# Optimization experiments

Measured on AMD Instinct MI355X. Metric: run time of the kernel, lower is better.

## Reference

```python
import jax, jax.numpy as jnp
import numpy as np

B_, L_, H_ = 8, 512, 768
DIN, N, R, K = 1536, 64, 48, 4  # d_inner, d_state, dt_rank, d_conv


def setup_inputs() -> dict:
    key = jax.random.key(0)
    ks = jax.random.split(key, 16)
    rn = lambda i, shp, sc=0.02: jax.random.normal(ks[i], shp, dtype=jnp.float32) * sc
    inp = {
        "text": jax.random.normal(ks[0], (B_, L_, H_), dtype=jnp.float32),
        "audio": jax.random.normal(ks[1], (B_, L_, H_), dtype=jnp.float32),
        "video": jax.random.normal(ks[2], (B_, L_, H_), dtype=jnp.float32),
        "proj_w": rn(3, (3 * H_, H_)),
        "proj_b": jnp.zeros((H_,), jnp.float32),
        "proj_ln_g": jnp.ones((H_,), jnp.float32),
        "proj_ln_b": jnp.zeros((H_,), jnp.float32),
        "blk_ln_g": jnp.ones((H_,), jnp.float32),
        "blk_ln_b": jnp.zeros((H_,), jnp.float32),
        "in_proj_w": rn(4, (H_, 2 * DIN)),
        "conv_w": rn(5, (DIN, 1, K), 0.1),
        "conv_b": jnp.zeros((DIN,), jnp.float32),
        "x_proj_w": rn(6, (DIN, R + 2 * N)),
        "dt_proj_w": rn(7, (R, DIN), 0.1),
        "dt_proj_b": jnp.full((DIN,), -4.6, jnp.float32),  # softplus -> ~0.01 dt
        "A_log": jnp.log(jnp.tile(jnp.arange(1, N + 1, dtype=jnp.float32), (DIN, 1))),
        "D": jnp.ones((DIN,), jnp.float32),
        "out_proj_w": rn(8, (DIN, H_)),
    }
    return inp


def _ln(x, g, b, eps=1e-5):
    mu = x.mean(-1, keepdims=True)
    xc = x - mu
    v = (xc * xc).mean(-1, keepdims=True)
    return xc * jax.lax.rsqrt(v + eps) * g + b


def _mamba(h, in_proj_w, conv_w, conv_b, x_proj_w, dt_proj_w, dt_proj_b, A_log, D, out_proj_w):
    Bsz, L, _ = h.shape
    xz = h @ in_proj_w                       # [B,L,2*DIN]
    x, z = jnp.split(xz, 2, axis=-1)         # each [B,L,DIN]
    # causal depthwise conv1d over time
    xc = jax.lax.conv_general_dilated(
        x.transpose(0, 2, 1), conv_w, (1,), [(K - 1, 0)],
        dimension_numbers=("NCH", "OIH", "NCH"), feature_group_count=DIN)
    x = jax.nn.silu(xc + conv_b[None, :, None]).transpose(0, 2, 1)  # [B,L,DIN]
    dbl = x @ x_proj_w                       # [B,L,R+2N]
    dt, Bm, Cm = jnp.split(dbl, [R, R + N], axis=-1)
    delta = jax.nn.softplus(dt @ dt_proj_w + dt_proj_b)  # [B,L,DIN]
    A = -jnp.exp(A_log)                      # [DIN,N]

    def step(hcar, t):
        d_t, b_t, c_t, u_t = t               # [B,DIN],[B,N],[B,N],[B,DIN]
        hcar = jnp.exp(d_t[..., None] * A) * hcar + (d_t * u_t)[..., None] * b_t[:, None, :]
        y = jnp.einsum("bdn,bn->bd", hcar, c_t)
        return hcar, y

    xs = (delta.transpose(1, 0, 2), Bm.transpose(1, 0, 2), Cm.transpose(1, 0, 2), x.transpose(1, 0, 2))
    h0 = jnp.zeros((Bsz, DIN, N), x.dtype)
    _, ys = jax.lax.scan(step, h0, xs)       # ys: [L,B,DIN]
    y = ys.transpose(1, 0, 2) + x * D
    y = y * jax.nn.silu(z)
    return y @ out_proj_w                    # [B,L,H]


def reference(text, audio, video, proj_w, proj_b, proj_ln_g, proj_ln_b,
              blk_ln_g, blk_ln_b, in_proj_w, conv_w, conv_b, x_proj_w,
              dt_proj_w, dt_proj_b, A_log, D, out_proj_w):
    fused = jnp.concatenate([text, audio, video], axis=-1) @ proj_w + proj_b
    fused = _ln(fused, proj_ln_g, proj_ln_b)
    m = _mamba(_ln(fused, blk_ln_g, blk_ln_b), in_proj_w, conv_w, conv_b,
               x_proj_w, dt_proj_w, dt_proj_b, A_log, D, out_proj_w)
    fused = fused + m                         # residual (dropout = identity in eval)
    return fused.mean(axis=1)                 # [B,H]
```

## Files before the change

kernel.cpp:

```cpp
#include <hip/hip_runtime.h>
#include <hip/hip_bf16.h>
#include <cstddef>
#include <cstdint>

#define DIN 1536
#define LSEQ 512

typedef __hip_bfloat16 bf16;
typedef __attribute__((ext_vector_type(8))) short short8x;
typedef __attribute__((ext_vector_type(4))) float f32x4;
typedef const __attribute__((address_space(1))) unsigned int* gp1;
typedef __attribute__((address_space(3))) unsigned int* lp3;

__device__ inline float readlane_f(float v, int l) {
  return __uint_as_float(__builtin_amdgcn_readlane(__float_as_uint(v), l));
}
__device__ inline void gload_lds(const bf16* g, unsigned short* l) {
  __builtin_amdgcn_global_load_lds((gp1)g, (lp3)l, 16, 0, 0);
}
__device__ inline void bsplit(float v, bf16& h, bf16& l) {
  h = __float2bfloat16(v);
  l = __float2bfloat16(v - __bfloat162float(h));
}
__device__ inline float softplusf(float t) {
  return fmaxf(t, 0.f) + log1pf(__expf(-fabsf(t)));
}
template<int CTRL>
__device__ inline float dpp_add(float v) {
  int t = __builtin_amdgcn_update_dpp(0, __float_as_int(v), CTRL, 0xf, 0xf, true);
  return v + __int_as_float(t);
}
__device__ inline float dpp_wave_sum(float p) {
  p = dpp_add<0x111>(p);
  p = dpp_add<0x112>(p);
  p = dpp_add<0x114>(p);
  p = dpp_add<0x118>(p);
  p = dpp_add<0x142>(p);
  p = dpp_add<0x143>(p);
  return p;
}

template<int TBM, int TBN, int WR, int WC, int AMODE, int EPI>
__global__ __launch_bounds__(WR*WC*64) void mgemm(
    const bf16* __restrict__ Ah0, const bf16* __restrict__ Al0,
    const bf16* __restrict__ Ah1, const bf16* __restrict__ Al1,
    const bf16* __restrict__ Ah2, const bf16* __restrict__ Al2,
    const bf16* __restrict__ Bh, const bf16* __restrict__ Bl,
    const float* __restrict__ bias,
    float* __restrict__ C, float* __restrict__ C2,
    bf16* __restrict__ Oh, bf16* __restrict__ Ol,
    int K, int lda, int ldc)
{
  constexpr int NW = WR * WC;
  constexpr int SM = TBM / WR, SN = TBN / WC;
  constexpr int T_M = SM / 16, T_N = SN / 16;
  __shared__ unsigned short sAh[TBM * 32], sAl[TBM * 32];
  __shared__ unsigned short sBh[TBN * 32], sBl[TBN * 32];
  const int tid = threadIdx.x;
  const int lane = tid & 63, wid = tid >> 6;
  const int bm = blockIdx.x * TBM, bn = blockIdx.y * TBN;
  const int wr = wid / WC, wc = wid % WC;

  const int stg_m = lane >> 2;
  const int stg_k = ((lane & 3) ^ ((lane >> 3) & 3)) * 8;
  const int fo = (lane & 15) * 64 + ((((lane >> 4) ^ ((lane >> 1) & 3)) & 3) * 16);

  f32x4 acc[T_M][T_N];
  #pragma unroll
  for (int i = 0; i < T_M; ++i)
    #pragma unroll
    for (int j = 0; j < T_N; ++j) acc[i][j] = (f32x4){0.f, 0.f, 0.f, 0.f};

  for (int k0 = 0; k0 < K; k0 += 32) {
    __syncthreads();
    const bf16* pAh; const bf16* pAl; int ka;
    if (AMODE == 1) {
      int seg = k0 / 768;
      pAh = (seg == 0) ? Ah0 : (seg == 1) ? Ah1 : Ah2;
      pAl = (seg == 0) ? Al0 : (seg == 1) ? Al1 : Al2;
      ka = k0 - seg * 768;
    } else { pAh = Ah0; pAl = Al0; ka = k0; }
    #pragma unroll
    for (int q = wid; q < TBM / 16; q += NW) {
      size_t go = (size_t)(bm + q * 16 + stg_m) * lda + ka + stg_k;
      gload_lds(pAh + go, &sAh[q * 512]);
      gload_lds(pAl + go, &sAl[q * 512]);
    }
    #pragma unroll
    for (int q = wid; q < TBN / 16; q += NW) {
      size_t go = (size_t)(bn + q * 16 + stg_m) * K + k0 + stg_k;
      gload_lds(Bh + go, &sBh[q * 512]);
      gload_lds(Bl + go, &sBl[q * 512]);
    }
    __syncthreads();

    short8x ah[T_M], al[T_M], bh[T_N], bl[T_N];
    #pragma unroll
    for (int mi = 0; mi < T_M; ++mi) {
      int off = (wr * SM + mi * 16) * 64 + fo;
      ah[mi] = *(const short8x*)((const char*)sAh + off);
      al[mi] = *(const short8x*)((const char*)sAl + off);
    }
    #pragma unroll
    for (int nj = 0; nj < T_N; ++nj) {
      int off = (wc * SN + nj * 16) * 64 + fo;
      bh[nj] = *(const short8x*)((const char*)sBh + off);
      bl[nj] = *(const short8x*)((const char*)sBl + off);
    }
    #pragma unroll
    for (int mi = 0; mi < T_M; ++mi)
      #pragma unroll
      for (int nj = 0; nj < T_N; ++nj) {
        acc[mi][nj] = __builtin_amdgcn_mfma_f32_16x16x32_bf16(ah[mi], bh[nj], acc[mi][nj], 0, 0, 0);
        acc[mi][nj] = __builtin_amdgcn_mfma_f32_16x16x32_bf16(ah[mi], bl[nj], acc[mi][nj], 0, 0, 0);
        acc[mi][nj] = __builtin_amdgcn_mfma_f32_16x16x32_bf16(al[mi], bh[nj], acc[mi][nj], 0, 0, 0);
      }
  }

  const int cl = lane & 15, qd = lane >> 4;
  const int colbase = bn + wc * SN;
  const int rowbase = bm + wr * SM;
  if (EPI == 1) {
    #pragma unroll
    for (int mi = 0; mi < T_M; ++mi) {
      int r0 = rowbase + mi * 16 + qd * 4;
      #pragma unroll
      for (int nj = 0; nj < T_N; ++nj) {
        int col = colbase + nj * 16 + cl;
        float bv = bias[col];
        #pragma unroll
        for (int rg = 0; rg < 4; ++rg)
          C[(size_t)(r0 + rg) * ldc + col] = acc[mi][nj][rg] + bv;
      }
    }
  } else if (EPI == 4) {
    #pragma unroll
    for (int mi = 0; mi < T_M; ++mi) {
      int m = rowbase + mi * 16 + qd * 4;
      int b = m >> 9, l = m & 511;
      #pragma unroll
      for (int nj = 0; nj < T_N; ++nj) {
        int col = colbase + nj * 16 + cl;
        float bv = bias[col];
        float4 v;
        v.x = softplusf(acc[mi][nj][0] + bv);
        v.y = softplusf(acc[mi][nj][1] + bv);
        v.z = softplusf(acc[mi][nj][2] + bv);
        v.w = softplusf(acc[mi][nj][3] + bv);
        *reinterpret_cast<float4*>(&C[((size_t)b * DIN + col) * LSEQ + l]) = v;
      }
    }
  } else if (EPI == 5) {
    if (bn < 1536) {
      #pragma unroll
      for (int mi = 0; mi < T_M; ++mi) {
        int r0 = rowbase + mi * 16 + qd * 4;
        #pragma unroll
        for (int nj = 0; nj < T_N; ++nj) {
          int col = colbase + nj * 16 + cl;
          #pragma unroll
          for (int rg = 0; rg < 4; ++rg)
            C[(size_t)(r0 + rg) * ldc + col] = acc[mi][nj][rg];
        }
      }
    } else {
      #pragma unroll
      for (int mi = 0; mi < T_M; ++mi) {
        int m = rowbase + mi * 16 + qd * 4;
        int b = m >> 9, l = m & 511;
        #pragma unroll
        for (int nj = 0; nj < T_N; ++nj) {
          int colz = colbase - 1536 + nj * 16 + cl;
          float4 v;
          v.x = acc[mi][nj][0]; v.y = acc[mi][nj][1];
          v.z = acc[mi][nj][2]; v.w = acc[mi][nj][3];
          *reinterpret_cast<float4*>(&C2[((size_t)b * DIN + colz) * LSEQ + l]) = v;
        }
      }
    }
  } else if (EPI == 6) {
    #pragma unroll
    for (int mi = 0; mi < T_M; ++mi) {
      int r0 = rowbase + mi * 16 + qd * 4;
      #pragma unroll
      for (int nj = 0; nj < T_N; ++nj) {
        int col = colbase + nj * 16 + cl;
        #pragma unroll
        for (int rg = 0; rg < 4; ++rg) {
          float v = acc[mi][nj][rg];
          C[(size_t)(r0 + rg) * 192 + col] = v;
          if (col < 64) {
            bf16 h, l;
            if (col < 48) bsplit(v, h, l);
            else { h = __float2bfloat16(0.f); l = h; }
            Oh[(size_t)(r0 + rg) * 64 + col] = h;
            Ol[(size_t)(r0 + rg) * 64 + col] = l;
          }
        }
      }
    }
  }
}

__global__ __launch_bounds__(256) void prep_k(
    const float* __restrict__ s0, const float* __restrict__ s1,
    const float* __restrict__ s2, bf16* __restrict__ moddst,
    const float* __restrict__ pw, const float* __restrict__ ipw,
    const float* __restrict__ xpw, const float* __restrict__ dtw,
    bf16* pwTh, bf16* pwTl, bf16* ipTh, bf16* ipTl,
    bf16* xpTh, bf16* xpTl, bf16* dtTh, bf16* dtTl)
{
  __shared__ float T[64][65];
  const int tid = threadIdx.x;
  if (blockIdx.x < 36864) {
    const int per = 4096 * 768 / 256;
    int seg = blockIdx.x / per;
    int idx = (blockIdx.x - seg * per) * 256 + tid;
    const float* src = (seg == 0) ? s0 : (seg == 1) ? s1 : s2;
    bf16* hi = moddst + (size_t)seg * 2 * 4096 * 768;
    bf16* lo = hi + (size_t)4096 * 768;
    bf16 h, l; bsplit(src[idx], h, l);
    hi[idx] = h; lo[idx] = l;
    return;
  }
  const int id = blockIdx.x - 36864;
  const float* src; bf16 *hi, *lo; int P, Q, ld, Ppad, px, qx;
  if (id < 432)       { src = pw;  hi = pwTh; lo = pwTl; P = 2304; Q = 768;  ld = 768;  Ppad = 2304; px = id % 36;          qx = id / 36; }
  else if (id < 1008) { int i = id - 432;  src = ipw; hi = ipTh; lo = ipTl; P = 768;  Q = 3072; ld = 3072; Ppad = 768;  px = i % 12; qx = i / 12; }
  else if (id < 1080) { int i = id - 1008; src = xpw; hi = xpTh; lo = xpTl; P = 1536; Q = 176;  ld = 176;  Ppad = 1536; px = i % 24; qx = i / 24; }
  else                { int i = id - 1080; src = dtw; hi = dtTh; lo = dtTl; P = 48;   Q = 1536; ld = 1536; Ppad = 64;   px = 0;      qx = i; }
  const int p0 = px * 64, q0 = qx * 64;
  {
    int j = tid & 63, i0 = tid >> 6;
    for (int i = i0; i < 64; i += 4) {
      int p = p0 + i, q = q0 + j;
      T[i][j] = (p < P && q < Q) ? src[(size_t)p * ld + q] : 0.f;
    }
  }
  __syncthreads();
  {
    int ii = tid & 63, j0 = tid >> 6;
    for (int jj = j0; jj < 64; jj += 4) {
      bf16 h, l; bsplit(T[ii][jj], h, l);
      size_t o = (size_t)(q0 + jj) * Ppad + p0 + ii;
      hi[o] = h; lo[o] = l;
    }
  }
}

__device__ inline float block_sum256(float s, float* red) {
  #pragma unroll
  for (int o = 32; o > 0; o >>= 1) s += __shfl_xor(s, o, 64);
  int tid = threadIdx.x;
  __syncthreads();
  if ((tid & 63) == 0) red[tid >> 6] = s;
  __syncthreads();
  return red[0] + red[1] + red[2] + red[3];
}

__global__ __launch_bounds__(256) void ln2_k(
    const float* __restrict__ pre,
    const float* __restrict__ g1, const float* __restrict__ b1,
    const float* __restrict__ g2, const float* __restrict__ b2,
    float* __restrict__ fused, bf16* __restrict__ hAh, bf16* __restrict__ hAl)
{
  __shared__ float red[4];
  const int row = blockIdx.x;
  const int tid = threadIdx.x;
  const float* x = pre + (size_t)row * 768;
  float v0 = x[tid], v1 = x[tid + 256], v2 = x[tid + 512];

  float mu = block_sum256(v0 + v1 + v2, red) * (1.f / 768.f);
  float c0 = v0 - mu, c1 = v1 - mu, c2 = v2 - mu;
  float var = block_sum256(c0*c0 + c1*c1 + c2*c2, red) * (1.f / 768.f);
  float r = rsqrtf(var + 1e-5f);
  float f0 = c0 * r * g1[tid] + b1[tid];
  float f1 = c1 * r * g1[tid + 256] + b1[tid + 256];
  float f2 = c2 * r * g1[tid + 512] + b1[tid + 512];
  float* fo = fused + (size_t)row * 768;
  fo[tid] = f0; fo[tid + 256] = f1; fo[tid + 512] = f2;

  float mu2 = block_sum256(f0 + f1 + f2, red) * (1.f / 768.f);
  float d0 = f0 - mu2, d1 = f1 - mu2, d2 = f2 - mu2;
  float var2 = block_sum256(d0*d0 + d1*d1 + d2*d2, red) * (1.f / 768.f);
  float r2 = rsqrtf(var2 + 1e-5f);
  float h0 = d0 * r2 * g2[tid] + b2[tid];
  float h1 = d1 * r2 * g2[tid + 256] + b2[tid + 256];
  float h2 = d2 * r2 * g2[tid + 512] + b2[tid + 512];
  bf16 hh, hl;
  size_t o = (size_t)row * 768;
  bsplit(h0, hh, hl); hAh[o + tid] = hh; hAl[o + tid] = hl;
  bsplit(h1, hh, hl); hAh[o + tid + 256] = hh; hAl[o + tid + 256] = hl;
  bsplit(h2, hh, hl); hAh[o + tid + 512] = hh; hAl[o + tid + 512] = hl;
}

__global__ __launch_bounds__(256) void conv2x_k(
    const float* __restrict__ xbuf, const float* __restrict__ w,
    const float* __restrict__ cb, float* __restrict__ xct,
    bf16* __restrict__ xcAh, bf16* __restrict__ xcAl)
{
  __shared__ float Xs[67][65];
  __shared__ float Ys[64][65];
  const int tid = threadIdx.x;
  const int l0 = blockIdx.x * 64;
  const int d0 = blockIdx.y * 64;
  const int b  = blockIdx.z;
  for (int e = tid; e < 67 * 64; e += 256) {
    int r = e >> 6, dd = e & 63;
    int l = l0 - 3 + r;
    Xs[r][dd] = (l >= 0) ? xbuf[((size_t)b * 512 + l) * DIN + d0 + dd] : 0.f;
  }
  __syncthreads();
  {
    const int lane = tid & 63, grp = tid >> 6;
    #pragma unroll
    for (int i = 0; i < 16; ++i) {
      int dd = grp + i * 4;
      int d = d0 + dd;
      float acc = cb[d];
      #pragma unroll
      for (int k = 0; k < 4; ++k)
        acc = fmaf(Xs[lane + k][dd], w[d * 4 + k], acc);
      float v = acc / (1.f + __expf(-acc));
      xct[((size_t)b * DIN + d) * LSEQ + l0 + lane] = v;
      Ys[lane][dd] = v;
    }
  }
  __syncthreads();
  {
    const int dd = tid & 63, lg = tid >> 6;
    #pragma unroll
    for (int j = 0; j < 16; ++j) {
      int l = lg * 16 + j;
      bf16 h, lo; bsplit(Ys[l][dd], h, lo);
      size_t o = (size_t)(b * 512 + l0 + l) * DIN + d0 + dd;
      xcAh[o] = h; xcAl[o] = lo;
    }
  }
}

__global__ __launch_bounds__(256) void scan5_k(
    const float* __restrict__ delta_t, const float* __restrict__ xct,
    const float* __restrict__ dbl, const float* __restrict__ zt,
    const float* __restrict__ A_log, const float* __restrict__ Dv,
    float* __restrict__ ysbar)
{
  __shared__ float BC[64][128];
  __shared__ float DT[4][64][2];
  __shared__ float Pq[4][64][17];
  const int tid = threadIdx.x;
  const int lane = tid & 63;
  const int wv = tid >> 6;
  const int bid = blockIdx.x;
  const int b = bid / 384;
  const int d = (bid - b * 384) * 4 + wv;
  const float Ad2 = -__expf(A_log[d * 64 + lane]) * 1.442695041f;
  const float Dd = Dv[d];
  const size_t strm = ((size_t)b * DIN + d) * LSEQ;
  float h = 0.f, ysum = 0.f;

  for (int l0 = 0; l0 < LSEQ; l0 += 64) {
    __syncthreads();
    #pragma unroll
    for (int i = 0; i < 16; ++i) {
      int t = wv * 16 + i;
      const float* src = dbl + (size_t)(b * LSEQ + l0 + t) * 192;
      float2 v; v.x = src[48 + lane]; v.y = src[112 + lane];
      *reinterpret_cast<float2*>(&BC[t][lane * 2]) = v;
    }
    float dt_v = delta_t[strm + l0 + lane];
    float u_v  = xct[strm + l0 + lane];
    float z_v  = zt[strm + l0 + lane];
    float2 dd; dd.x = dt_v; dd.y = dt_v * u_v;
    *reinterpret_cast<float2*>(&DT[wv][lane][0]) = dd;
    __syncthreads();

    #pragma unroll
    for (int t = 0; t < 64; ++t) {
      float2 sd = *reinterpret_cast<const float2*>(&DT[wv][t][0]);
      float2 bc = *reinterpret_cast<const float2*>(&BC[t][lane * 2]);
      float e = exp2f(sd.x * Ad2);
      h = fmaf(e, h, sd.y * bc.x);
      float p = h * bc.y;
      p = dpp_add<0x111>(p);
      p = dpp_add<0x112>(p);
      if ((lane & 3) == 3) Pq[wv][t][lane >> 2] = p;
    }
    float yk = 0.f;
    #pragma unroll
    for (int j = 0; j < 16; ++j) yk += Pq[wv][lane][j];
    float yv = (yk + u_v * Dd) * (z_v / (1.f + __expf(-z_v)));
    ysum += yv;
  }
  float tot = readlane_f(dpp_wave_sum(ysum), 63);
  if (lane == 0) ysbar[b * 1536 + d] = tot;
}

__global__ __launch_bounds__(256) void final_k(
    const float* __restrict__ fused, const float* __restrict__ ysbar,
    const float* __restrict__ W, float* __restrict__ out)
{
  __shared__ float ys[1536];
  const int b = blockIdx.y;
  const int c = blockIdx.x * 256 + threadIdx.x;
  for (int i = threadIdx.x; i < 1536; i += 256) ys[i] = ysbar[b * 1536 + i];
  __syncthreads();
  float sf = 0.f;
  for (int l = 0; l < 512; ++l) sf += fused[(size_t)((b << 9) + l) * 768 + c];
  float dot = 0.f;
  for (int d = 0; d < 1536; ++d) dot = fmaf(ys[d], W[(size_t)d * 768 + c], dot);
  out[b * 768 + c] = (sf + dot) * (1.f / 512.f);
}

extern "C" void kernel_launch(void* const* d_in, const int* in_sizes, int n_in,
                              void* d_out, int out_size, void* d_ws, size_t ws_size,
                              hipStream_t stream)
{
  const float* text      = (const float*)d_in[0];
  const float* audio     = (const float*)d_in[1];
  const float* video     = (const float*)d_in[2];
  const float* proj_w    = (const float*)d_in[3];
  const float* proj_b    = (const float*)d_in[4];
  const float* proj_ln_g = (const float*)d_in[5];
  const float* proj_ln_b = (const float*)d_in[6];
  const float* blk_ln_g  = (const float*)d_in[7];
  const float* blk_ln_b  = (const float*)d_in[8];
  const float* in_proj_w = (const float*)d_in[9];
  const float* conv_w    = (const float*)d_in[10];
  const float* conv_b    = (const float*)d_in[11];
  const float* x_proj_w  = (const float*)d_in[12];
  const float* dt_proj_w = (const float*)d_in[13];
  const float* dt_proj_b = (const float*)d_in[14];
  const float* A_log     = (const float*)d_in[15];
  const float* Dv        = (const float*)d_in[16];
  const float* out_projw = (const float*)d_in[17];
  float* out = (float*)d_out;

  char* p = (char*)d_ws;
  const size_t P768 = (size_t)4096 * 768 * 2;
  char* S1 = p; p += 6 * P768;
  char* SW = p; p += 18087936;
  char* S3 = p; p += (size_t)4096 * 768 * 4;
  char* S4 = p; p += (size_t)4096 * 768 * 4;
  char* S6 = p; p += (size_t)4096 * 1536 * 4;
  char* S7 = p; p += (size_t)4096 * 1536 * 4;
  char* S8 = p; p += (size_t)4096 * 1536 * 4;
  char* SD = p; p += (size_t)4096 * 64 * 4;
  char* S9 = p; p += (size_t)4096 * 192 * 4;
  char* SY = p; p += 12288 * 4;

  bf16* modspl = (bf16*)S1;
  bf16 *tAh = (bf16*)S1,              *tAl = (bf16*)(S1 + P768);
  bf16 *aAh = (bf16*)(S1 + 2 * P768), *aAl = (bf16*)(S1 + 3 * P768);
  bf16 *vAh = (bf16*)(S1 + 4 * P768), *vAl = (bf16*)(S1 + 5 * P768);
  bf16 *hAh = (bf16*)S1,              *hAl = (bf16*)(S1 + P768);
  bf16 *xcAh = (bf16*)S1,             *xcAl = (bf16*)(S1 + (size_t)4096 * 1536 * 2);
  bf16 *pwTh = (bf16*)SW,                    *pwTl = pwTh + (size_t)768 * 2304;
  bf16 *ipTh = pwTl + (size_t)768 * 2304,    *ipTl = ipTh + (size_t)3072 * 768;
  bf16 *xpTh = ipTl + (size_t)3072 * 768,    *xpTl = xpTh + (size_t)192 * 1536;
  bf16 *dtTh = xpTl + (size_t)192 * 1536,    *dtTl = dtTh + (size_t)1536 * 64;
  float* pre     = (float*)S3;
  float* fused   = (float*)S4;
  float* xbuf    = (float*)S6;  float* delta_t = (float*)S6;
  float* zt      = (float*)S7;
  float* xct     = (float*)S8;
  bf16 *dtAh = (bf16*)SD, *dtAl = (bf16*)(SD + (size_t)4096 * 64 * 2);
  float* dbl     = (float*)S9;
  float* ysbar   = (float*)SY;

  prep_k<<<37968, 256, 0, stream>>>(text, audio, video, modspl,
                                    proj_w, in_proj_w, x_proj_w, dt_proj_w,
                                    pwTh, pwTl, ipTh, ipTl, xpTh, xpTl, dtTh, dtTl);
  mgemm<128, 64, 4, 2, 1, 1><<<dim3(32, 12), 512, 0, stream>>>(
      tAh, tAl, aAh, aAl, vAh, vAl, pwTh, pwTl, proj_b,
      pre, nullptr, nullptr, nullptr, 2304, 768, 768);
  ln2_k<<<4096, 256, 0, stream>>>(pre, proj_ln_g, proj_ln_b, blk_ln_g, blk_ln_b, fused, hAh, hAl);
  mgemm<128, 128, 2, 2, 0, 5><<<dim3(32, 24), 256, 0, stream>>>(
      hAh, hAl, nullptr, nullptr, nullptr, nullptr, ipTh, ipTl, nullptr,
      xbuf, zt, nullptr, nullptr, 768, 768, 1536);
  conv2x_k<<<dim3(8, 24, 8), 256, 0, stream>>>(xbuf, conv_w, conv_b, xct, xcAh, xcAl);
  mgemm<64, 64, 4, 2, 0, 6><<<dim3(64, 3), 512, 0, stream>>>(
      xcAh, xcAl, nullptr, nullptr, nullptr, nullptr, xpTh, xpTl, nullptr,
      dbl, nullptr, dtAh, dtAl, 1536, 1536, 192);
  mgemm<128, 64, 4, 2, 0, 4><<<dim3(32, 24), 512, 0, stream>>>(
      dtAh, dtAl, nullptr, nullptr, nullptr, nullptr, dtTh, dtTl, dt_proj_b,
      delta_t, nullptr, nullptr, nullptr, 64, 64, 0);
  scan5_k<<<3072, 256, 0, stream>>>(delta_t, xct, dbl, zt, A_log, Dv, ysbar);
  final_k<<<dim3(3, 8), 256, 0, stream>>>(fused, ysbar, out_projw, out);
}
```

Before: 663.7 us.

## Fold gate and time-sum into scan accumulator, drop per-step y reduction

The scan kernel no longer builds y_t per timestep through DPP reductions and an LDS transpose. It uses linearity of the time-mean: each lane accumulates h*C*silu(z) directly into one scalar, and the wave is reduced once at the end. The per-step dt, dt*u and gate scalars are broadcast with readlane instead of LDS reads. Blocks grow to 8 waves so the B/C tile loaded into LDS is shared by more channels. The cost is a different summation order, plus three readlanes and an extra multiply per step.

```diff
diff --git a/kernel.cpp b/kernel.cpp
--- a/kernel.cpp
+++ b/kernel.cpp
@@ -339,31 +339,31 @@
   }
 }
 
-__global__ __launch_bounds__(256) void scan5_k(
+__global__ __launch_bounds__(512) void scan6_k(
     const float* __restrict__ delta_t, const float* __restrict__ xct,
     const float* __restrict__ dbl, const float* __restrict__ zt,
     const float* __restrict__ A_log, const float* __restrict__ Dv,
     float* __restrict__ ysbar)
 {
   __shared__ float BC[64][128];
-  __shared__ float DT[4][64][2];
-  __shared__ float Pq[4][64][17];
   const int tid = threadIdx.x;
   const int lane = tid & 63;
   const int wv = tid >> 6;
   const int bid = blockIdx.x;
-  const int b = bid / 384;
-  const int d = (bid - b * 384) * 4 + wv;
+  const int b = bid / 192;
+  const int d = (bid - b * 192) * 8 + wv;
   const float Ad2 = -__expf(A_log[d * 64 + lane]) * 1.442695041f;
   const float Dd = Dv[d];
   const size_t strm = ((size_t)b * DIN + d) * LSEQ;
-  float h = 0.f, ysum = 0.f;
+  float h = 0.f;
+  float a = 0.f;
+  float us = 0.f;
 
   for (int l0 = 0; l0 < LSEQ; l0 += 64) {
     __syncthreads();
     #pragma unroll
-    for (int i = 0; i < 16; ++i) {
-      int t = wv * 16 + i;
+    for (int i = 0; i < 8; ++i) {
+      int t = wv * 8 + i;
       const float* src = dbl + (size_t)(b * LSEQ + l0 + t) * 192;
       float2 v; v.x = src[48 + lane]; v.y = src[112 + lane];
       *reinterpret_cast<float2*>(&BC[t][lane * 2]) = v;
@@ -371,28 +371,23 @@
     float dt_v = delta_t[strm + l0 + lane];
     float u_v  = xct[strm + l0 + lane];
     float z_v  = zt[strm + l0 + lane];
-    float2 dd; dd.x = dt_v; dd.y = dt_v * u_v;
-    *reinterpret_cast<float2*>(&DT[wv][lane][0]) = dd;
+    float du_v = dt_v * u_v;
+    float sz_v = z_v / (1.f + __expf(-z_v));
+    us += u_v * sz_v;
     __syncthreads();
 
     #pragma unroll
     for (int t = 0; t < 64; ++t) {
-      float2 sd = *reinterpret_cast<const float2*>(&DT[wv][t][0]);
+      float sdt = readlane_f(dt_v, t);
+      float sdu = readlane_f(du_v, t);
+      float ssz = readlane_f(sz_v, t);
       float2 bc = *reinterpret_cast<const float2*>(&BC[t][lane * 2]);
-      float e = exp2f(sd.x * Ad2);
-      h = fmaf(e, h, sd.y * bc.x);
-      float p = h * bc.y;
-      p = dpp_add<0x111>(p);
-      p = dpp_add<0x112>(p);
-      if ((lane & 3) == 3) Pq[wv][t][lane >> 2] = p;
-    }
-    float yk = 0.f;
-    #pragma unroll
-    for (int j = 0; j < 16; ++j) yk += Pq[wv][lane][j];
-    float yv = (yk + u_v * Dd) * (z_v / (1.f + __expf(-z_v)));
-    ysum += yv;
-  }
-  float tot = readlane_f(dpp_wave_sum(ysum), 63);
+      float e = exp2f(sdt * Ad2);
+      h = fmaf(e, h, sdu * bc.x);
+      a = fmaf(h, bc.y * ssz, a);
+    }
+  }
+  float tot = readlane_f(dpp_wave_sum(a + Dd * us), 63);
   if (lane == 0) ysbar[b * 1536 + d] = tot;
 }
 
@@ -485,6 +480,6 @@
   mgemm<128, 64, 4, 2, 0, 4><<<dim3(32, 24), 512, 0, stream>>>(
       dtAh, dtAl, nullptr, nullptr, nullptr, nullptr, dtTh, dtTl, dt_proj_b,
       delta_t, nullptr, nullptr, nullptr, 64, 64, 0);
-  scan5_k<<<3072, 256, 0, stream>>>(delta_t, xct, dbl, zt, A_log, Dv, ysbar);
+  scan6_k<<<1536, 512, 0, stream>>>(delta_t, xct, dbl, zt, A_log, Dv, ysbar);
   final_k<<<dim3(3, 8), 256, 0, stream>>>(fused, ysbar, out_projw, out);
 }
```

After: 615.8 us. 1.08x faster.
